# Optimization experiments

Hardware: AMD Instinct MI355X
Metric: run time of the kernel (lower is better)

## Reference

```python
import jax, jax.numpy as jnp
import numpy as np

B, L, D_MODEL, D_STATE, D_HIDDEN = 4, 4096, 1024, 256, 4096
RMIN, RMAX, MAX_PHASE = 0.8, 0.95, 2.0 * np.pi


def setup_inputs() -> dict:
    key = jax.random.key(0)
    ks = jax.random.split(key, 10)
    # LRU ring init (Orvieto et al.): |lambda| in [rmin, rmax], phase in [0, max_phase)
    u1 = jax.random.uniform(ks[0], (D_STATE,))
    u2 = jax.random.uniform(ks[1], (D_STATE,))
    nu_log = jnp.log(-0.5 * jnp.log(u1 * (RMAX**2 - RMIN**2) + RMIN**2))
    theta_log = jnp.log(MAX_PHASE * u2)
    B_re = jax.random.normal(ks[2], (D_STATE, D_MODEL)) / np.sqrt(2.0 * D_MODEL)
    B_im = jax.random.normal(ks[3], (D_STATE, D_MODEL)) / np.sqrt(2.0 * D_MODEL)
    C_re = jax.random.normal(ks[4], (D_MODEL, D_STATE)) / np.sqrt(D_STATE)
    C_im = jax.random.normal(ks[5], (D_MODEL, D_STATE)) / np.sqrt(D_STATE)
    D_mat = jax.random.normal(ks[6], (D_MODEL, D_MODEL)) / np.sqrt(D_MODEL)
    W1 = jax.random.normal(ks[7], (D_MODEL, D_HIDDEN)) * np.sqrt(2.0 / D_MODEL)
    W2 = jax.random.normal(ks[8], (D_HIDDEN, D_MODEL)) * np.sqrt(2.0 / D_HIDDEN)
    res_logit = jnp.asarray(-1.0, dtype=jnp.float32)
    x3d = jax.random.normal(ks[9], (B, L, D_MODEL), dtype=jnp.float32)
    return {"x3d": x3d, "nu_log": nu_log, "theta_log": theta_log,
            "B_re": B_re, "B_im": B_im, "C_re": C_re, "C_im": C_im,
            "D_mat": D_mat, "W1": W1, "W2": W2, "res_logit": res_logit}


def _lru_scan(lam, Bu):
    # diagonal linear recurrence x_t = lam * x_{t-1} + Bu_t via associative scan
    lam_b = jnp.broadcast_to(lam, Bu.shape)  # [B, L, N]

    def comb(a, b):
        return (a[0] * b[0], b[0] * a[1] + b[1])

    _, states = jax.lax.associative_scan(comb, (lam_b, Bu), axis=1)
    return states  # [B, L, N] complex


def reference(x3d, nu_log, theta_log, B_re, B_im, C_re, C_im, D_mat, W1, W2, res_logit):
    lam = jnp.exp(-jnp.exp(nu_log) + 1j * jnp.exp(theta_log))          # [N]
    gamma = jnp.sqrt(1.0 - jnp.abs(lam) ** 2)                           # [N]
    Bn = (gamma[:, None] * (B_re + 1j * B_im))                          # [N, D]
    Bu = jnp.einsum('bld,nd->bln', x3d.astype(jnp.complex64), Bn)       # [B, L, N]
    states = _lru_scan(lam.astype(jnp.complex64), Bu)                   # [B, L, N]
    y = jnp.einsum('bln,mn->blm', states, C_re + 1j * C_im).real \
        + jnp.einsum('bld,md->blm', x3d, D_mat)                         # [B, L, D]
    # MLP feedforward (nl_layers=2, bias=False), dropout is identity at p=0
    z = jax.nn.gelu(y @ W1) @ W2                                        # [B, L, D]
    out = x3d + jax.nn.sigmoid(res_logit) * z
    st = states[:, -1]  # final recurrent state
    return out, st
```

## Files before the change

### kernel.cpp

```cpp
#include <hip/hip_runtime.h>
#include <stdint.h>

typedef __bf16 bf16;
typedef bf16 bf16x8 __attribute__((ext_vector_type(8)));
typedef float f32x4 __attribute__((ext_vector_type(4)));

#define B_  4
#define L_  4096
#define DM  1024
#define DS  256
#define DH  4096
#define BL  16384
#define CL  64
#define NC  64

__device__ __forceinline__ float bfbits(uint32_t lo16) {
  union { uint32_t u; float f; } v; v.u = lo16 << 16; return v.f;
}

__device__ __forceinline__ void async16(const bf16* g, bf16* l) {
  __builtin_amdgcn_global_load_lds(
      (const __attribute__((address_space(1))) uint32_t*)g,
      (__attribute__((address_space(3))) uint32_t*)l, 16, 0, 0);
}

#define MEMFENCE()  asm volatile("" ::: "memory")
#define LGKM0()     asm volatile("s_waitcnt lgkmcnt(0)" ::: "memory")
#define SCHEDB()    __builtin_amdgcn_sched_barrier(0)

__global__ void phaseA(const float* __restrict__ nu_log,
                       const float* __restrict__ th_log,
                       float* __restrict__ scal) {
  int n = threadIdx.x;
  float nu = __expf(nu_log[n]);
  float th = __expf(th_log[n]);
  float mod = __expf(-nu);
  float lr = mod * cosf(th);
  float li = mod * sinf(th);
  float g = sqrtf(fmaxf(1.0f - mod * mod, 0.0f));
  float pr = 1.f, pi = 0.f;
  for (int i = 0; i < CL; i++) {
    float nr = pr * lr - pi * li;
    float ni = pr * li + pi * lr;
    pr = nr; pi = ni;
  }
  scal[n] = lr; scal[256 + n] = li;
  scal[512 + n] = pr; scal[768 + n] = pi;
  scal[1024 + n] = g;
}

__global__ void prep_bu(const float* __restrict__ B_re, const float* __restrict__ B_im,
                        const float* __restrict__ scal, bf16* __restrict__ WB) {
  size_t i = (size_t)blockIdx.x * 256 + threadIdx.x;
  int row = (int)(i >> 10), col = (int)(i & 1023);
  int n = row >> 1;
  const float* src = (row & 1) ? B_im : B_re;
  WB[i] = (bf16)(scal[1024 + n] * src[n * 1024 + col]);
}

__global__ void prep_y(const float* __restrict__ C_re, const float* __restrict__ C_im,
                       const float* __restrict__ D_mat, bf16* __restrict__ WB) {
  size_t i = (size_t)blockIdx.x * 256 + threadIdx.x;
  int m = (int)(i / 1536), c = (int)(i % 1536);
  float v;
  if (c < 256)       v = C_re[m * 256 + c];
  else if (c < 512)  v = -C_im[m * 256 + (c - 256)];
  else               v = D_mat[m * 1024 + (c - 512)];
  WB[i] = (bf16)v;
}

__global__ void transpose_to_bf16(const float* __restrict__ in, bf16* __restrict__ out,
                                  int R, int C) {
  __shared__ float tile[32][33];
  int c0 = blockIdx.x * 32, r0 = blockIdx.y * 32;
  int tx = threadIdx.x, ty = threadIdx.y;
  for (int i = 0; i < 32; i += 8)
    tile[ty + i][tx] = in[(size_t)(r0 + ty + i) * C + c0 + tx];
  __syncthreads();
  for (int i = 0; i < 32; i += 8)
    out[(size_t)(c0 + ty + i) * R + r0 + tx] = (bf16)tile[tx][ty + i];
}

__global__ void conv_x(const float4* __restrict__ x, bf16* __restrict__ XS) {
  size_t i = (size_t)blockIdx.x * 256 + threadIdx.x;
  size_t t = i >> 8;
  int d4 = (int)(i & 255);
  float4 v = x[i];
  bf16* o = XS + t * 1536 + 512 + (size_t)d4 * 4;
  o[0] = (bf16)v.x; o[1] = (bf16)v.y; o[2] = (bf16)v.z; o[3] = (bf16)v.w;
}

template <int EPI>
__device__ __forceinline__ void epi_store(void* C, int ldc, size_t row, size_t col,
                                          float v, float sig, const float* xres) {
  size_t off = row * (size_t)ldc + col;
  if (EPI == 0) {
    ((bf16*)C)[off] = (bf16)v;
  } else if (EPI == 1) {
    float z = 0.7978845608f * (v + 0.044715f * v * v * v);
    float gv = v / (1.f + __expf(-2.f * z));
    ((bf16*)C)[off] = (bf16)gv;
  } else {
    ((float*)C)[off] = xres[off] + sig * v;
  }
}

template <int EPI>
__global__ __launch_bounds__(512, 2) void gemm256(
    const bf16* __restrict__ A, int lda,
    const bf16* __restrict__ Bt, int ldb,
    void* __restrict__ C, int ldc, int NK, int mt, int nt,
    const float* __restrict__ xres, const float* __restrict__ reslog) {
  __shared__ __align__(16) bf16 sA[2 * 16384];
  __shared__ __align__(16) bf16 sB[2 * 16384];

  const int tid  = threadIdx.x;
  const int lane = tid & 63;
  const int wave = tid >> 6;
  const int q = lane >> 4, l16 = lane & 15;
  const int wr = wave >> 2, wc = wave & 3;

  int nb = mt * nt;
  int per = nb >> 3;
  int t0 = (blockIdx.x & 7) * per + (blockIdx.x >> 3);
  int gsz = nt << 3;
  int g = t0 / gsz, r = t0 % gsz;
  size_t m0 = (size_t)(g * 8 + (r & 7)) * 256;
  size_t n0 = (size_t)(r >> 3) * 256;

  const int srow = tid >> 3;
  const int scol = (((tid & 7) ^ ((tid >> 3) & 7)) << 3);
  const bf16* gA = A  + (m0 + srow) * (size_t)lda + scol;
  const bf16* gB = Bt + (n0 + srow) * (size_t)ldb + scol;
  bf16* lA = sA + tid * 8;
  bf16* lB = sB + tid * 8;

  auto stageA = [&](int kt) {
    const bf16* s = gA + kt * 64;
    bf16* l = lA + (kt & 1) * 16384;
    async16(s, l);
    async16(s + (size_t)64  * lda, l + 4096);
    async16(s + (size_t)128 * lda, l + 8192);
    async16(s + (size_t)192 * lda, l + 12288);
  };
  auto stageB = [&](int kt) {
    const bf16* s = gB + kt * 64;
    bf16* l = lB + (kt & 1) * 16384;
    async16(s, l);
    async16(s + (size_t)64  * ldb, l + 4096);
    async16(s + (size_t)128 * ldb, l + 8192);
    async16(s + (size_t)192 * ldb, l + 12288);
  };

  stageA(0); stageB(0); stageA(1); stageB(1);
  __builtin_amdgcn_s_waitcnt(0x0F78);
  __builtin_amdgcn_s_barrier();
  MEMFENCE();

  const int sw  = (l16 & 7) << 3;
  const int qx0 = (q << 3) ^ sw;
  const int qx1 = ((q << 3) + 32) ^ sw;
  const bf16* Ard = sA + wr * 8192 + l16 * 64;
  const bf16* Brd = sB + (wc >> 1) * 8192 + ((wc & 1) * 64 + l16) * 64;

  f32x4 acc[8][4] = {};
  bf16x8 a0[4], a1[4], b0[4], b1[4];

#pragma unroll
  for (int j = 0; j < 4; ++j) a0[j] = *(const bf16x8*)&Ard[j * 1024 + qx0];
#pragma unroll
  for (int n = 0; n < 4; ++n) b0[n] = *(const bf16x8*)&Brd[n * 1024 + qx0];

  for (int kt = 0; kt < NK; ++kt) {
    const bf16* Ab  = Ard + (kt & 1) * 16384;
    const bf16* Bb  = Brd + (kt & 1) * 16384;
    const bf16* Abn = Ard + ((kt + 1) & 1) * 16384;
    const bf16* Bbn = Brd + ((kt + 1) & 1) * 16384;

#pragma unroll
    for (int j = 0; j < 4; ++j) a1[j] = *(const bf16x8*)&Ab[j * 1024 + qx1];
#pragma unroll
    for (int n = 0; n < 4; ++n) b1[n] = *(const bf16x8*)&Bb[n * 1024 + qx1];
    SCHEDB();
    __builtin_amdgcn_s_setprio(1);
#pragma unroll
    for (int j = 0; j < 4; ++j)
#pragma unroll
      for (int n = 0; n < 4; ++n)
        acc[j][n] = __builtin_amdgcn_mfma_f32_16x16x32_bf16(a0[j], b0[n], acc[j][n], 0, 0, 0);
    __builtin_amdgcn_s_setprio(0);

#pragma unroll
    for (int j = 0; j < 4; ++j) a0[j] = *(const bf16x8*)&Ab[(4 + j) * 1024 + qx0];
    SCHEDB();
    __builtin_amdgcn_s_setprio(1);
#pragma unroll
    for (int j = 0; j < 4; ++j)
#pragma unroll
      for (int n = 0; n < 4; ++n)
        acc[j][n] = __builtin_amdgcn_mfma_f32_16x16x32_bf16(a1[j], b1[n], acc[j][n], 0, 0, 0);
    __builtin_amdgcn_s_setprio(0);

#pragma unroll
    for (int j = 0; j < 4; ++j) a1[j] = *(const bf16x8*)&Ab[(4 + j) * 1024 + qx1];
    SCHEDB();
    __builtin_amdgcn_s_setprio(1);
#pragma unroll
    for (int j = 0; j < 4; ++j)
#pragma unroll
      for (int n = 0; n < 4; ++n)
        acc[4 + j][n] = __builtin_amdgcn_mfma_f32_16x16x32_bf16(a0[j], b0[n], acc[4 + j][n], 0, 0, 0);
    __builtin_amdgcn_s_setprio(0);

    MEMFENCE();
    __builtin_amdgcn_s_waitcnt(0x0F70);
    LGKM0();
    __builtin_amdgcn_s_barrier();
    MEMFENCE();

    if (kt + 1 < NK) {
#pragma unroll
      for (int j = 0; j < 4; ++j) a0[j] = *(const bf16x8*)&Abn[j * 1024 + qx0];
#pragma unroll
      for (int n = 0; n < 4; ++n) b0[n] = *(const bf16x8*)&Bbn[n * 1024 + qx0];
    }
    if (kt + 2 < NK) { stageA(kt + 2); stageB(kt + 2); }
    SCHEDB();
    __builtin_amdgcn_s_setprio(1);
#pragma unroll
    for (int j = 0; j < 4; ++j)
#pragma unroll
      for (int n = 0; n < 4; ++n)
        acc[4 + j][n] = __builtin_amdgcn_mfma_f32_16x16x32_bf16(a1[j], b1[n], acc[4 + j][n], 0, 0, 0);
    __builtin_amdgcn_s_setprio(0);
  }

  float sig = 0.f;
  if (EPI == 2) sig = 1.f / (1.f + __expf(-reslog[0]));
#pragma unroll
  for (int mi = 0; mi < 8; ++mi)
#pragma unroll
    for (int ni = 0; ni < 4; ++ni) {
      size_t col = n0 + wc * 64 + ni * 16 + l16;
#pragma unroll
      for (int r2 = 0; r2 < 4; ++r2) {
        size_t row = m0 + wr * 128 + mi * 16 + q * 4 + r2;
        epi_store<EPI>(C, ldc, row, col, acc[mi][ni][r2], sig, xres);
      }
    }
}

template <int EPI>
__global__ __launch_bounds__(512, 2) void gemm128(
    const bf16* __restrict__ A, int lda,
    const bf16* __restrict__ Bt, int ldb,
    void* __restrict__ C, int ldc, int NK, int mt, int nt,
    const float* __restrict__ xres, const float* __restrict__ reslog) {
  __shared__ __align__(16) bf16 sA[2 * 8192];
  __shared__ __align__(16) bf16 sB[2 * 16384];

  const int tid  = threadIdx.x;
  const int lane = tid & 63;
  const int wave = tid >> 6;
  const int q = lane >> 4, l16 = lane & 15;
  const int wr = wave >> 2, wc = wave & 3;

  int nb = mt * nt;
  int per = nb >> 3;
  int t0 = (blockIdx.x & 7) * per + (blockIdx.x >> 3);
  int gsz = nt << 3;
  int g = t0 / gsz, r = t0 % gsz;
  size_t m0 = (size_t)(g * 8 + (r & 7)) * 128;
  size_t n0 = (size_t)(r >> 3) * 256;

  const int srow = tid >> 3;
  const int scol = (((tid & 7) ^ ((tid >> 3) & 7)) << 3);
  const bf16* gA = A  + (m0 + srow) * (size_t)lda + scol;
  const bf16* gB = Bt + (n0 + srow) * (size_t)ldb + scol;
  bf16* lA = sA + tid * 8;
  bf16* lB = sB + tid * 8;

  auto stageA = [&](int kt) {
    const bf16* s = gA + kt * 64;
    bf16* l = lA + (kt & 1) * 8192;
    async16(s, l);
    async16(s + (size_t)64 * lda, l + 4096);
  };
  auto stageB = [&](int kt) {
    const bf16* s = gB + kt * 64;
    bf16* l = lB + (kt & 1) * 16384;
    async16(s, l);
    async16(s + (size_t)64  * ldb, l + 4096);
    async16(s + (size_t)128 * ldb, l + 8192);
    async16(s + (size_t)192 * ldb, l + 12288);
  };

  stageA(0); stageB(0); stageA(1); stageB(1);
  __builtin_amdgcn_s_waitcnt(0x0F76);
  __builtin_amdgcn_s_barrier();
  MEMFENCE();

  const int sw  = (l16 & 7) << 3;
  const int qx0 = (q << 3) ^ sw;
  const int qx1 = ((q << 3) + 32) ^ sw;
  const bf16* Ard = sA + (wr * 64 + l16) * 64;
  const bf16* Brd = sB + (wc >> 1) * 8192 + ((wc & 1) * 64 + l16) * 64;

  f32x4 acc[4][4] = {};
  bf16x8 a0[4], a1[4], b0[4], b1[4];

#pragma unroll
  for (int j = 0; j < 4; ++j) a0[j] = *(const bf16x8*)&Ard[j * 1024 + qx0];
#pragma unroll
  for (int n = 0; n < 4; ++n) b0[n] = *(const bf16x8*)&Brd[n * 1024 + qx0];

  for (int kt = 0; kt < NK; ++kt) {
    const bf16* Ab  = Ard + (kt & 1) * 8192;
    const bf16* Bb  = Brd + (kt & 1) * 16384;
    const bf16* Abn = Ard + ((kt + 1) & 1) * 8192;
    const bf16* Bbn = Brd + ((kt + 1) & 1) * 16384;

#pragma unroll
    for (int j = 0; j < 4; ++j) a1[j] = *(const bf16x8*)&Ab[j * 1024 + qx1];
#pragma unroll
    for (int n = 0; n < 4; ++n) b1[n] = *(const bf16x8*)&Bb[n * 1024 + qx1];
    SCHEDB();
    __builtin_amdgcn_s_setprio(1);
#pragma unroll
    for (int j = 0; j < 4; ++j)
#pragma unroll
      for (int n = 0; n < 4; ++n)
        acc[j][n] = __builtin_amdgcn_mfma_f32_16x16x32_bf16(a0[j], b0[n], acc[j][n], 0, 0, 0);
    __builtin_amdgcn_s_setprio(0);

    MEMFENCE();
    __builtin_amdgcn_s_waitcnt(0x0F70);
    LGKM0();
    __builtin_amdgcn_s_barrier();
    MEMFENCE();

    if (kt + 1 < NK) {
#pragma unroll
      for (int j = 0; j < 4; ++j) a0[j] = *(const bf16x8*)&Abn[j * 1024 + qx0];
#pragma unroll
      for (int n = 0; n < 4; ++n) b0[n] = *(const bf16x8*)&Bbn[n * 1024 + qx0];
    }
    if (kt + 2 < NK) { stageA(kt + 2); stageB(kt + 2); }
    SCHEDB();
    __builtin_amdgcn_s_setprio(1);
#pragma unroll
    for (int j = 0; j < 4; ++j)
#pragma unroll
      for (int n = 0; n < 4; ++n)
        acc[j][n] = __builtin_amdgcn_mfma_f32_16x16x32_bf16(a1[j], b1[n], acc[j][n], 0, 0, 0);
    __builtin_amdgcn_s_setprio(0);
  }

  float sig = 0.f;
  if (EPI == 2) sig = 1.f / (1.f + __expf(-reslog[0]));
#pragma unroll
  for (int mi = 0; mi < 4; ++mi)
#pragma unroll
    for (int ni = 0; ni < 4; ++ni) {
      size_t col = n0 + wc * 64 + ni * 16 + l16;
#pragma unroll
      for (int r2 = 0; r2 < 4; ++r2) {
        size_t row = m0 + wr * 64 + mi * 16 + q * 4 + r2;
        epi_store<EPI>(C, ldc, row, col, acc[mi][ni][r2], sig, xres);
      }
    }
}

__global__ void scan_pass1(const bf16* __restrict__ Bu, const float* __restrict__ scal,
                           float2* __restrict__ H) {
  int b = blockIdx.x >> 6, c = blockIdx.x & 63, n = threadIdx.x;
  float lr = scal[n], li = scal[256 + n];
  float sr = 0.f, si = 0.f;
  size_t t0 = (size_t)b * L_ + (size_t)c * CL;
  const uint32_t* p = (const uint32_t*)(Bu + t0 * 512) + n;
  for (int j = 0; j < CL; j++) {
    uint32_t u = p[(size_t)j * 256];
    float ur = bfbits(u & 0xffffu), ui = bfbits(u >> 16);
    float nr = lr * sr - li * si + ur;
    float ni = lr * si + li * sr + ui;
    sr = nr; si = ni;
  }
  H[(size_t)(b * NC + c) * 256 + n] = make_float2(sr, si);
}

__global__ void scan_pass2(const float2* __restrict__ H, const float* __restrict__ scal,
                           float2* __restrict__ Carry) {
  int b = blockIdx.x, n = threadIdx.x;
  float Pr = scal[512 + n], Pi = scal[768 + n];
  float cr = 0.f, ci = 0.f;
  for (int c = 0; c < NC; c++) {
    Carry[(size_t)(b * NC + c) * 256 + n] = make_float2(cr, ci);
    float2 h = H[(size_t)(b * NC + c) * 256 + n];
    float nr = Pr * cr - Pi * ci + h.x;
    float ni = Pr * ci + Pi * cr + h.y;
    cr = nr; ci = ni;
  }
}

__global__ void scan_pass3(const bf16* __restrict__ Bu, const float* __restrict__ scal,
                           const float2* __restrict__ Carry, bf16* __restrict__ XS,
                           float* __restrict__ st) {
  int b = blockIdx.x >> 6, c = blockIdx.x & 63, n = threadIdx.x;
  float lr = scal[n], li = scal[256 + n];
  float2 cv = Carry[(size_t)(b * NC + c) * 256 + n];
  float sr = cv.x, si = cv.y;
  size_t t0 = (size_t)b * L_ + (size_t)c * CL;
  const uint32_t* p = (const uint32_t*)(Bu + t0 * 512) + n;
  bf16* qp = XS + t0 * 1536 + n;
  for (int j = 0; j < CL; j++) {
    uint32_t u = p[(size_t)j * 256];
    float ur = bfbits(u & 0xffffu), ui = bfbits(u >> 16);
    float nr = lr * sr - li * si + ur;
    float ni = lr * si + li * sr + ui;
    sr = nr; si = ni;
    qp[(size_t)j * 1536] = (bf16)sr;
    qp[(size_t)j * 1536 + 256] = (bf16)si;
  }
  if (c == NC - 1) {
    st[(size_t)b * 256 + n] = sr;
    st[1024 + (size_t)b * 256 + n] = si;
  }
}

extern "C" void kernel_launch(void* const* d_in, const int* in_sizes, int n_in,
                              void* d_out, int out_size, void* d_ws, size_t ws_size,
                              hipStream_t stream) {
  const float* x      = (const float*)d_in[0];
  const float* nu_log = (const float*)d_in[1];
  const float* th_log = (const float*)d_in[2];
  const float* B_re   = (const float*)d_in[3];
  const float* B_im   = (const float*)d_in[4];
  const float* C_re   = (const float*)d_in[5];
  const float* C_im   = (const float*)d_in[6];
  const float* D_mat  = (const float*)d_in[7];
  const float* W1     = (const float*)d_in[8];
  const float* W2     = (const float*)d_in[9];
  const float* reslog = (const float*)d_in[10];

  char* wsb = (char*)d_ws;
  size_t off = 0;
  auto alloc = [&](size_t bytes) {
    void* p = wsb + off;
    off += (bytes + 255) & ~(size_t)255;
    return p;
  };
  float*  scal = (float*)alloc(5 * 256 * 4);
  bf16*   WBbu = (bf16*)alloc((size_t)512 * 1024 * 2);
  bf16*   WBy  = (bf16*)alloc((size_t)1024 * 1536 * 2);
  bf16*   WB1  = (bf16*)alloc((size_t)4096 * 1024 * 2);
  bf16*   WB2  = (bf16*)alloc((size_t)1024 * 4096 * 2);
  float2* H    = (float2*)alloc((size_t)B_ * NC * 256 * 8);
  float2* Cr   = (float2*)alloc((size_t)B_ * NC * 256 * 8);
  bf16*   Ybf  = (bf16*)alloc((size_t)BL * 1024 * 2);
  bf16*   XS   = (bf16*)alloc((size_t)BL * 1536 * 2);
  bf16*   Bu   = (bf16*)alloc((size_t)BL * 512 * 2);
  bf16*   Hbf  = XS;

  float* out = (float*)d_out;
  float* st  = out + (size_t)BL * DM;

  phaseA<<<1, 256, 0, stream>>>(nu_log, th_log, scal);
  prep_bu<<<512 * 1024 / 256, 256, 0, stream>>>(B_re, B_im, scal, WBbu);
  prep_y<<<1024 * 1536 / 256, 256, 0, stream>>>(C_re, C_im, D_mat, WBy);
  transpose_to_bf16<<<dim3(4096 / 32, 1024 / 32), dim3(32, 8), 0, stream>>>(W1, WB1, 1024, 4096);
  transpose_to_bf16<<<dim3(1024 / 32, 4096 / 32), dim3(32, 8), 0, stream>>>(W2, WB2, 4096, 1024);
  conv_x<<<BL * 256 / 256, 256, 0, stream>>>((const float4*)x, XS);

  gemm128<0><<<128 * 2, 512, 0, stream>>>(
      XS + 512, 1536, WBbu, 1024, Bu, 512, 16, 128, 2, nullptr, nullptr);

  scan_pass1<<<B_ * NC, 256, 0, stream>>>(Bu, scal, H);
  scan_pass2<<<B_, 256, 0, stream>>>(H, scal, Cr);
  scan_pass3<<<B_ * NC, 256, 0, stream>>>(Bu, scal, Cr, XS, st);

  gemm256<0><<<64 * 4, 512, 0, stream>>>(
      XS, 1536, WBy, 1536, Ybf, 1024, 24, 64, 4, nullptr, nullptr);

  for (int i = 0; i < 2; i++) {
    const bf16* Yc = Ybf + (size_t)i * 8192 * 1024;
    float* Oc = out + (size_t)i * 8192 * 1024;
    const float* Xc = x + (size_t)i * 8192 * 1024;
    gemm256<1><<<32 * 16, 512, 0, stream>>>(
        Yc, 1024, WB1, 1024, Hbf, 4096, 16, 32, 16, nullptr, nullptr);
    gemm128<2><<<64 * 4, 512, 0, stream>>>(
        Hbf, 4096, WB2, 4096, Oc, 1024, 64, 64, 4, Xc, reslog);
  }
}
```

Baseline: 555.9 us.

## Fuse prep kernels into one launch and interleave GEMM LDS reads with MFMAs

The six small preprocessing kernels (lambda scalars, B/C/D weight packing, W1/W2 transposes, x conversion) are merged into one block-dispatched kernel, and the gamma factor is recomputed inline so it no longer depends on the scalar kernel. Both GEMM main loops are restructured into regA/regB halves with peeled final iterations. Hard sched_barriers are replaced by sched_group_barrier patterns that interleave LDS reads and global-to-LDS staging with MFMA groups. The aim is to cut launch overhead and hide LDS latency behind matrix ops, at the cost of relying on compiler scheduling hints and longer code.

```diff
diff --git a/kernel.cpp b/kernel.cpp
--- a/kernel.cpp
+++ b/kernel.cpp
@@ -26,68 +26,71 @@
 
 #define MEMFENCE()  asm volatile("" ::: "memory")
 #define LGKM0()     asm volatile("s_waitcnt lgkmcnt(0)" ::: "memory")
-#define SCHEDB()    __builtin_amdgcn_sched_barrier(0)
-
-__global__ void phaseA(const float* __restrict__ nu_log,
-                       const float* __restrict__ th_log,
-                       float* __restrict__ scal) {
-  int n = threadIdx.x;
-  float nu = __expf(nu_log[n]);
-  float th = __expf(th_log[n]);
-  float mod = __expf(-nu);
-  float lr = mod * cosf(th);
-  float li = mod * sinf(th);
-  float g = sqrtf(fmaxf(1.0f - mod * mod, 0.0f));
-  float pr = 1.f, pi = 0.f;
-  for (int i = 0; i < CL; i++) {
-    float nr = pr * lr - pi * li;
-    float ni = pr * li + pi * lr;
-    pr = nr; pi = ni;
-  }
-  scal[n] = lr; scal[256 + n] = li;
-  scal[512 + n] = pr; scal[768 + n] = pi;
-  scal[1024 + n] = g;
-}
-
-__global__ void prep_bu(const float* __restrict__ B_re, const float* __restrict__ B_im,
-                        const float* __restrict__ scal, bf16* __restrict__ WB) {
-  size_t i = (size_t)blockIdx.x * 256 + threadIdx.x;
-  int row = (int)(i >> 10), col = (int)(i & 1023);
-  int n = row >> 1;
-  const float* src = (row & 1) ? B_im : B_re;
-  WB[i] = (bf16)(scal[1024 + n] * src[n * 1024 + col]);
-}
-
-__global__ void prep_y(const float* __restrict__ C_re, const float* __restrict__ C_im,
-                       const float* __restrict__ D_mat, bf16* __restrict__ WB) {
-  size_t i = (size_t)blockIdx.x * 256 + threadIdx.x;
-  int m = (int)(i / 1536), c = (int)(i % 1536);
-  float v;
-  if (c < 256)       v = C_re[m * 256 + c];
-  else if (c < 512)  v = -C_im[m * 256 + (c - 256)];
-  else               v = D_mat[m * 1024 + (c - 512)];
-  WB[i] = (bf16)v;
-}
-
-__global__ void transpose_to_bf16(const float* __restrict__ in, bf16* __restrict__ out,
-                                  int R, int C) {
+#define MFMA16(a, b, c) __builtin_amdgcn_mfma_f32_16x16x32_bf16((a), (b), (c), 0, 0, 0)
+#define SGB(mask, n) __builtin_amdgcn_sched_group_barrier((mask), (n), 0)
+
+__global__ void prep_fused(const float4* __restrict__ x, bf16* __restrict__ XS,
+                           const float* __restrict__ C_re, const float* __restrict__ C_im,
+                           const float* __restrict__ D_mat, bf16* __restrict__ WBy,
+                           const float* __restrict__ B_re, const float* __restrict__ B_im,
+                           const float* __restrict__ nu_log, const float* __restrict__ th_log,
+                           bf16* __restrict__ WBbu,
+                           const float* __restrict__ W1, bf16* __restrict__ WB1,
+                           const float* __restrict__ W2, bf16* __restrict__ WB2,
+                           float* __restrict__ scal) {
   __shared__ float tile[32][33];
-  int c0 = blockIdx.x * 32, r0 = blockIdx.y * 32;
-  int tx = threadIdx.x, ty = threadIdx.y;
-  for (int i = 0; i < 32; i += 8)
-    tile[ty + i][tx] = in[(size_t)(r0 + ty + i) * C + c0 + tx];
-  __syncthreads();
-  for (int i = 0; i < 32; i += 8)
-    out[(size_t)(c0 + ty + i) * R + r0 + tx] = (bf16)tile[tx][ty + i];
-}
-
-__global__ void conv_x(const float4* __restrict__ x, bf16* __restrict__ XS) {
-  size_t i = (size_t)blockIdx.x * 256 + threadIdx.x;
-  size_t t = i >> 8;
-  int d4 = (int)(i & 255);
-  float4 v = x[i];
-  bf16* o = XS + t * 1536 + 512 + (size_t)d4 * 4;
-  o[0] = (bf16)v.x; o[1] = (bf16)v.y; o[2] = (bf16)v.z; o[3] = (bf16)v.w;
+  int bid = blockIdx.x, tid = threadIdx.x;
+  if (bid < 16384) {
+    size_t i = (size_t)bid * 256 + tid;
+    size_t t = i >> 8;
+    int d4 = (int)(i & 255);
+    float4 v = x[i];
+    bf16* o = XS + t * 1536 + 512 + (size_t)d4 * 4;
+    o[0] = (bf16)v.x; o[1] = (bf16)v.y; o[2] = (bf16)v.z; o[3] = (bf16)v.w;
+  } else if (bid < 22528) {
+    size_t i = (size_t)(bid - 16384) * 256 + tid;
+    int m = (int)(i / 1536), c = (int)(i % 1536);
+    float v;
+    if (c < 256)       v = C_re[m * 256 + c];
+    else if (c < 512)  v = -C_im[m * 256 + (c - 256)];
+    else               v = D_mat[m * 1024 + (c - 512)];
+    WBy[i] = (bf16)v;
+  } else if (bid < 24576) {
+    size_t i = (size_t)(bid - 22528) * 256 + tid;
+    int row = (int)(i >> 10), col = (int)(i & 1023);
+    int n = row >> 1;
+    float mod = __expf(-__expf(nu_log[n]));
+    float g = sqrtf(fmaxf(1.0f - mod * mod, 0.0f));
+    const float* src = (row & 1) ? B_im : B_re;
+    WBbu[i] = (bf16)(g * src[n * 1024 + col]);
+  } else if (bid < 32768) {
+    const float* in; bf16* out; int R, C, bx, by;
+    if (bid < 28672) { int t = bid - 24576; in = W1; out = WB1; R = 1024; C = 4096; bx = t & 127; by = t >> 7; }
+    else             { int t = bid - 28672; in = W2; out = WB2; R = 4096; C = 1024; bx = t & 31;  by = t >> 5; }
+    int c0 = bx * 32, r0 = by * 32, tx = tid & 31, ty = tid >> 5;
+    for (int i = 0; i < 32; i += 8)
+      tile[ty + i][tx] = in[(size_t)(r0 + ty + i) * C + c0 + tx];
+    __syncthreads();
+    for (int i = 0; i < 32; i += 8)
+      out[(size_t)(c0 + ty + i) * R + r0 + tx] = (bf16)tile[tx][ty + i];
+  } else {
+    int n = tid;
+    float nu = __expf(nu_log[n]);
+    float th = __expf(th_log[n]);
+    float mod = __expf(-nu);
+    float lr = mod * cosf(th);
+    float li = mod * sinf(th);
+    float g = sqrtf(fmaxf(1.0f - mod * mod, 0.0f));
+    float pr = 1.f, pi = 0.f;
+    for (int i = 0; i < CL; i++) {
+      float nr = pr * lr - pi * li;
+      float ni = pr * li + pi * lr;
+      pr = nr; pi = ni;
+    }
+    scal[n] = lr; scal[256 + n] = li;
+    scal[512 + n] = pr; scal[768 + n] = pi;
+    scal[1024 + n] = g;
+  }
 }
 
 template <int EPI>
@@ -105,6 +108,15 @@
   }
 }
 
+#define SYNC256()                                   \
+  do {                                              \
+    MEMFENCE();                                     \
+    __builtin_amdgcn_s_waitcnt(0x0F70);             \
+    LGKM0();                                        \
+    __builtin_amdgcn_s_barrier();                   \
+    MEMFENCE();                                     \
+  } while (0)
+
 template <int EPI>
 __global__ __launch_bounds__(512, 2) void gemm256(
     const bf16* __restrict__ A, int lda,
@@ -171,68 +183,88 @@
 #pragma unroll
   for (int n = 0; n < 4; ++n) b0[n] = *(const bf16x8*)&Brd[n * 1024 + qx0];
 
-  for (int kt = 0; kt < NK; ++kt) {
+  auto regA = [&](const bf16* Ab, const bf16* Bb) {
+#pragma unroll
+    for (int j = 0; j < 4; ++j) a1[j] = *(const bf16x8*)&Ab[j * 1024 + qx1];
+#pragma unroll
+    for (int n = 0; n < 4; ++n) b1[n] = *(const bf16x8*)&Bb[n * 1024 + qx1];
+#pragma unroll
+    for (int j = 0; j < 4; ++j)
+#pragma unroll
+      for (int n = 0; n < 4; ++n)
+        acc[j][n] = MFMA16(a0[j], b0[n], acc[j][n]);
+#pragma unroll
+    for (int j = 0; j < 4; ++j) a0[j] = *(const bf16x8*)&Ab[(4 + j) * 1024 + qx0];
+#pragma unroll
+    for (int j = 0; j < 4; ++j)
+#pragma unroll
+      for (int n = 0; n < 4; ++n)
+        acc[j][n] = MFMA16(a1[j], b1[n], acc[j][n]);
+#pragma unroll
+    for (int j = 0; j < 4; ++j) a1[j] = *(const bf16x8*)&Ab[(4 + j) * 1024 + qx1];
+#pragma unroll
+    for (int j = 0; j < 4; ++j)
+#pragma unroll
+      for (int n = 0; n < 4; ++n)
+        acc[4 + j][n] = MFMA16(a0[j], b0[n], acc[4 + j][n]);
+#pragma unroll
+    for (int g2 = 0; g2 < 8; ++g2) { SGB(0x100, 2); SGB(0x008, 4); }
+#pragma unroll
+    for (int g2 = 0; g2 < 4; ++g2) SGB(0x008, 4);
+  };
+
+  auto regB = [&](const bf16* Abn, const bf16* Bbn) {
+#pragma unroll
+    for (int j = 0; j < 4; ++j) a0[j] = *(const bf16x8*)&Abn[j * 1024 + qx0];
+#pragma unroll
+    for (int n = 0; n < 4; ++n) b0[n] = *(const bf16x8*)&Bbn[n * 1024 + qx0];
+#pragma unroll
+    for (int j = 0; j < 4; ++j)
+#pragma unroll
+      for (int n = 0; n < 4; ++n)
+        acc[4 + j][n] = MFMA16(a1[j], b1[n], acc[4 + j][n]);
+  };
+
+  for (int kt = 0; kt < NK - 2; ++kt) {
     const bf16* Ab  = Ard + (kt & 1) * 16384;
     const bf16* Bb  = Brd + (kt & 1) * 16384;
     const bf16* Abn = Ard + ((kt + 1) & 1) * 16384;
     const bf16* Bbn = Brd + ((kt + 1) & 1) * 16384;
 
-#pragma unroll
-    for (int j = 0; j < 4; ++j) a1[j] = *(const bf16x8*)&Ab[j * 1024 + qx1];
-#pragma unroll
-    for (int n = 0; n < 4; ++n) b1[n] = *(const bf16x8*)&Bb[n * 1024 + qx1];
-    SCHEDB();
     __builtin_amdgcn_s_setprio(1);
-#pragma unroll
-    for (int j = 0; j < 4; ++j)
-#pragma unroll
-      for (int n = 0; n < 4; ++n)
-        acc[j][n] = __builtin_amdgcn_mfma_f32_16x16x32_bf16(a0[j], b0[n], acc[j][n], 0, 0, 0);
+    regA(Ab, Bb);
     __builtin_amdgcn_s_setprio(0);
-
-#pragma unroll
-    for (int j = 0; j < 4; ++j) a0[j] = *(const bf16x8*)&Ab[(4 + j) * 1024 + qx0];
-    SCHEDB();
+    SYNC256();
     __builtin_amdgcn_s_setprio(1);
-#pragma unroll
-    for (int j = 0; j < 4; ++j)
-#pragma unroll
-      for (int n = 0; n < 4; ++n)
-        acc[j][n] = __builtin_amdgcn_mfma_f32_16x16x32_bf16(a1[j], b1[n], acc[j][n], 0, 0, 0);
+    stageA(kt + 2); stageB(kt + 2);
+    regB(Abn, Bbn);
+#pragma unroll
+    for (int g2 = 0; g2 < 4; ++g2) { SGB(0x100, 2); SGB(0x030, 2); SGB(0x008, 4); }
     __builtin_amdgcn_s_setprio(0);
-
-#pragma unroll
-    for (int j = 0; j < 4; ++j) a1[j] = *(const bf16x8*)&Ab[(4 + j) * 1024 + qx1];
-    SCHEDB();
-    __builtin_amdgcn_s_setprio(1);
-#pragma unroll
-    for (int j = 0; j < 4; ++j)
-#pragma unroll
-      for (int n = 0; n < 4; ++n)
-        acc[4 + j][n] = __builtin_amdgcn_mfma_f32_16x16x32_bf16(a0[j], b0[n], acc[4 + j][n], 0, 0, 0);
-    __builtin_amdgcn_s_setprio(0);
-
-    MEMFENCE();
-    __builtin_amdgcn_s_waitcnt(0x0F70);
-    LGKM0();
-    __builtin_amdgcn_s_barrier();
-    MEMFENCE();
-
-    if (kt + 1 < NK) {
-#pragma unroll
-      for (int j = 0; j < 4; ++j) a0[j] = *(const bf16x8*)&Abn[j * 1024 + qx0];
-#pragma unroll
-      for (int n = 0; n < 4; ++n) b0[n] = *(const bf16x8*)&Bbn[n * 1024 + qx0];
-    }
-    if (kt + 2 < NK) { stageA(kt + 2); stageB(kt + 2); }
-    SCHEDB();
-    __builtin_amdgcn_s_setprio(1);
-#pragma unroll
-    for (int j = 0; j < 4; ++j)
-#pragma unroll
-      for (int n = 0; n < 4; ++n)
-        acc[4 + j][n] = __builtin_amdgcn_mfma_f32_16x16x32_bf16(a1[j], b1[n], acc[4 + j][n], 0, 0, 0);
-    __builtin_amdgcn_s_setprio(0);
+  }
+
+  {
+    const int kt = NK - 2;
+    const bf16* Ab  = Ard + (kt & 1) * 16384;
+    const bf16* Bb  = Brd + (kt & 1) * 16384;
+    const bf16* Abn = Ard + ((kt + 1) & 1) * 16384;
+    const bf16* Bbn = Brd + ((kt + 1) & 1) * 16384;
+    regA(Ab, Bb);
+    SYNC256();
+    regB(Abn, Bbn);
+#pragma unroll
+    for (int g2 = 0; g2 < 4; ++g2) { SGB(0x100, 2); SGB(0x008, 4); }
+  }
+  {
+    const int kt = NK - 1;
+    const bf16* Ab = Ard + (kt & 1) * 16384;
+    const bf16* Bb = Brd + (kt & 1) * 16384;
+    regA(Ab, Bb);
+#pragma unroll
+    for (int j = 0; j < 4; ++j)
+#pragma unroll
+      for (int n = 0; n < 4; ++n)
+        acc[4 + j][n] = MFMA16(a1[j], b1[n], acc[4 + j][n]);
   }
 
   float sig = 0.f;
@@ -314,46 +346,71 @@
 #pragma unroll
   for (int n = 0; n < 4; ++n) b0[n] = *(const bf16x8*)&Brd[n * 1024 + qx0];
 
-  for (int kt = 0; kt < NK; ++kt) {
+  auto regA = [&](const bf16* Ab, const bf16* Bb) {
+#pragma unroll
+    for (int j = 0; j < 4; ++j) a1[j] = *(const bf16x8*)&Ab[j * 1024 + qx1];
+#pragma unroll
+    for (int n = 0; n < 4; ++n) b1[n] = *(const bf16x8*)&Bb[n * 1024 + qx1];
+#pragma unroll
+    for (int j = 0; j < 4; ++j)
+#pragma unroll
+      for (int n = 0; n < 4; ++n)
+        acc[j][n] = MFMA16(a0[j], b0[n], acc[j][n]);
+#pragma unroll
+    for (int g2 = 0; g2 < 4; ++g2) { SGB(0x100, 2); SGB(0x008, 4); }
+  };
+  auto regB = [&](const bf16* Abn, const bf16* Bbn) {
+#pragma unroll
+    for (int j = 0; j < 4; ++j) a0[j] = *(const bf16x8*)&Abn[j * 1024 + qx0];
+#pragma unroll
+    for (int n = 0; n < 4; ++n) b0[n] = *(const bf16x8*)&Bbn[n * 1024 + qx0];
+#pragma unroll
+    for (int j = 0; j < 4; ++j)
+#pragma unroll
+      for (int n = 0; n < 4; ++n)
+        acc[j][n] = MFMA16(a1[j], b1[n], acc[j][n]);
+  };
+
+  for (int kt = 0; kt < NK - 2; ++kt) {
     const bf16* Ab  = Ard + (kt & 1) * 8192;
     const bf16* Bb  = Brd + (kt & 1) * 16384;
     const bf16* Abn = Ard + ((kt + 1) & 1) * 8192;
     const bf16* Bbn = Brd + ((kt + 1) & 1) * 16384;
 
-#pragma unroll
-    for (int j = 0; j < 4; ++j) a1[j] = *(const bf16x8*)&Ab[j * 1024 + qx1];
-#pragma unroll
-    for (int n = 0; n < 4; ++n) b1[n] = *(const bf16x8*)&Bb[n * 1024 + qx1];
-    SCHEDB();
     __builtin_amdgcn_s_setprio(1);
-#pragma unroll
-    for (int j = 0; j < 4; ++j)
-#pragma unroll
-      for (int n = 0; n < 4; ++n)
-        acc[j][n] = __builtin_amdgcn_mfma_f32_16x16x32_bf16(a0[j], b0[n], acc[j][n], 0, 0, 0);
+    regA(Ab, Bb);
     __builtin_amdgcn_s_setprio(0);
-
-    MEMFENCE();
-    __builtin_amdgcn_s_waitcnt(0x0F70);
-    LGKM0();
-    __builtin_amdgcn_s_barrier();
-    MEMFENCE();
-
-    if (kt + 1 < NK) {
-#pragma unroll
-      for (int j = 0; j < 4; ++j) a0[j] = *(const bf16x8*)&Abn[j * 1024 + qx0];
-#pragma unroll
-      for (int n = 0; n < 4; ++n) b0[n] = *(const bf16x8*)&Bbn[n * 1024 + qx0];
-    }
-    if (kt + 2 < NK) { stageA(kt + 2); stageB(kt + 2); }
-    SCHEDB();
+    SYNC256();
     __builtin_amdgcn_s_setprio(1);
-#pragma unroll
-    for (int j = 0; j < 4; ++j)
-#pragma unroll
-      for (int n = 0; n < 4; ++n)
-        acc[j][n] = __builtin_amdgcn_mfma_f32_16x16x32_bf16(a1[j], b1[n], acc[j][n], 0, 0, 0);
+    stageA(kt + 2); stageB(kt + 2);
+    regB(Abn, Bbn);
+#pragma unroll
+    for (int g2 = 0; g2 < 3; ++g2) { SGB(0x100, 2); SGB(0x030, 2); SGB(0x008, 4); }
+    SGB(0x100, 2); SGB(0x008, 4);
     __builtin_amdgcn_s_setprio(0);
+  }
+  {
+    const int kt = NK - 2;
+    const bf16* Ab  = Ard + (kt & 1) * 8192;
+    const bf16* Bb  = Brd + (kt & 1) * 16384;
+    const bf16* Abn = Ard + ((kt + 1) & 1) * 8192;
+    const bf16* Bbn = Brd + ((kt + 1) & 1) * 16384;
+    regA(Ab, Bb);
+    SYNC256();
+    regB(Abn, Bbn);
+#pragma unroll
+    for (int g2 = 0; g2 < 4; ++g2) { SGB(0x100, 2); SGB(0x008, 4); }
+  }
+  {
+    const int kt = NK - 1;
+    const bf16* Ab = Ard + (kt & 1) * 8192;
+    const bf16* Bb = Brd + (kt & 1) * 16384;
+    regA(Ab, Bb);
+#pragma unroll
+    for (int j = 0; j < 4; ++j)
+#pragma unroll
+      for (int n = 0; n < 4; ++n)
+        acc[j][n] = MFMA16(a1[j], b1[n], acc[j][n]);
   }
 
   float sig = 0.f;
@@ -464,12 +521,9 @@
   float* out = (float*)d_out;
   float* st  = out + (size_t)BL * DM;
 
-  phaseA<<<1, 256, 0, stream>>>(nu_log, th_log, scal);
-  prep_bu<<<512 * 1024 / 256, 256, 0, stream>>>(B_re, B_im, scal, WBbu);
-  prep_y<<<1024 * 1536 / 256, 256, 0, stream>>>(C_re, C_im, D_mat, WBy);
-  transpose_to_bf16<<<dim3(4096 / 32, 1024 / 32), dim3(32, 8), 0, stream>>>(W1, WB1, 1024, 4096);
-  transpose_to_bf16<<<dim3(1024 / 32, 4096 / 32), dim3(32, 8), 0, stream>>>(W2, WB2, 4096, 1024);
-  conv_x<<<BL * 256 / 256, 256, 0, stream>>>((const float4*)x, XS);
+  prep_fused<<<32769, 256, 0, stream>>>(
+      (const float4*)x, XS, C_re, C_im, D_mat, WBy,
+      B_re, B_im, nu_log, th_log, WBbu, W1, WB1, W2, WB2, scal);
 
   gemm128<0><<<128 * 2, 512, 0, stream>>>(
       XS + 512, 1536, WBbu, 1024, Bu, 512, 16, 128, 2, nullptr, nullptr);
```

Result: slower. 587.3 us (+5.7%).
